# Performance work log

Hardware: AMD Instinct MI355X
Metric: run time of the kernel (lower is better)

The kernel has to match this reference:

```python
import jax, jax.numpy as jnp
import numpy as np

B, P, K, H, C = 8, 4096, 20, 64, 40  # clouds, points/cloud, knn k, hidden_feat, num_classes
NEG = 0.2  # LeakyReLU negative slope used by the repo MLP


def setup_inputs() -> dict:
    key = jax.random.key(0)
    ks = jax.random.split(key, 16)
    w = lambda k, shape: (jax.random.normal(k, shape, jnp.float32) / np.sqrt(shape[0]))
    return {
        "x": jax.random.normal(ks[0], (B * P, 3), jnp.float32),
        "batch": jnp.repeat(jnp.arange(B, dtype=jnp.int32), P),
        "W1": w(ks[1], (2 * 3, H)), "b1": jnp.zeros((H,), jnp.float32),
        "W2": w(ks[2], (2 * H, H)), "b2": jnp.zeros((H,), jnp.float32),
        "W3": w(ks[3], (2 * H, H)), "b3": jnp.zeros((H,), jnp.float32),
        "Wl": w(ks[4], (3 * H, 1024)), "bl": jnp.zeros((1024,), jnp.float32),
        "Wm1": w(ks[5], (1024, 256)), "bm1": jnp.zeros((256,), jnp.float32),
        "Wm2": w(ks[6], (256, 128)), "bm2": jnp.zeros((128,), jnp.float32),
        "Wo": w(ks[7], (128, C)), "bo": jnp.zeros((C,), jnp.float32),
    }


def _knn_idx(x):
    # x: [B,P,d] -> indices of K nearest neighbors (excluding self): [B,P,K]
    d2 = jnp.sum(x * x, axis=-1)  # [B,P]
    dist = d2[:, :, None] + d2[:, None, :] - 2.0 * jnp.einsum('bpd,bqd->bpq', x, x)
    dist = dist + jnp.eye(x.shape[1], dtype=x.dtype) * 1e10  # mask self-loops
    return jax.lax.top_k(-dist, K)[1]


def _edge_conv(x, W, b):
    # DynamicEdgeConv with max aggregation: nn([x_i, x_j - x_i]) maxed over K neighbors
    idx = _knn_idx(x)                                    # [B,P,K]
    x_j = jax.vmap(lambda xb, ib: xb[ib])(x, idx)        # [B,P,K,d]
    x_i = jnp.broadcast_to(x[:, :, None, :], x_j.shape)  # [B,P,K,d]
    feat = jnp.concatenate([x_i, x_j - x_i], axis=-1)    # [B,P,K,2d]
    h = jax.nn.leaky_relu(feat @ W + b, NEG)             # [B,P,K,H]
    return jnp.max(h, axis=2)                            # [B,P,H]


def reference(x, batch, W1, b1, W2, b2, W3, b3, Wl, bl, Wm1, bm1, Wm2, bm2, Wo, bo):
    # batch is sorted with equal-size clouds -> reshape to [B,P,3]
    xb = x.reshape(B, P, 3)
    x1 = _edge_conv(xb, W1, b1)
    x2 = _edge_conv(x1, W2, b2)
    x3 = _edge_conv(x2, W3, b3)
    h = jnp.concatenate([x1, x2, x3], axis=-1)           # [B,P,3H]
    h = jax.nn.leaky_relu(h @ Wl + bl, NEG)
    h = jax.nn.leaky_relu(h @ Wm1 + bm1, NEG)            # dropout = identity (eval)
    h = jax.nn.leaky_relu(h @ Wm2 + bm2, NEG)
    out = h @ Wo + bo                                    # [B,P,C]
    return jax.nn.log_softmax(out, axis=-1).reshape(B * P, C)
```

## Files before the change

### kernel.cpp

```cpp
#include <hip/hip_runtime.h>
#include <cstddef>
#include <cstdint>

constexpr int B_ = 8, P_ = 4096, K_ = 20, H_ = 64, C_ = 40;
constexpr int NPT = B_ * P_;
#define NEG_SLOPE 0.2f

typedef unsigned long long u64;
typedef unsigned int u32;
typedef unsigned short u16;
typedef __attribute__((ext_vector_type(8))) short bf16x8;
typedef __attribute__((ext_vector_type(4))) float f32x4;

__device__ inline u16 f2bf(float v) {
    u32 bits = __float_as_uint(v);
    return (u16)((bits + 0x7FFFu + ((bits >> 16) & 1)) >> 16);
}
__device__ inline float bf2f(u16 h) { return __uint_as_float((u32)h << 16); }

__device__ __forceinline__ void bubble20f(float (&a)[K_], float key) {
    float carry = key;
#pragma unroll
    for (int s = 0; s < K_; ++s) {
        float as = a[s];
        a[s]  = fminf(carry, as);
        carry = fmaxf(carry, as);
    }
}
__device__ __forceinline__ float mkkey(float dist, int cid) {
    return __uint_as_float((__float_as_uint(dist) & 0xFFFFF000u) | (u32)cid);
}

template <int D>
__global__ __launch_bounds__(256) void d2_kernel(const float* __restrict__ x,
                                                 float* __restrict__ d2) {
    int i = blockIdx.x * 256 + threadIdx.x;
    if (i >= NPT) return;
    const float* r = x + (size_t)i * D;
    float s = 0.f;
#pragma unroll
    for (int d = 0; d < D; ++d) { float v = r[d]; s += v * v; }
    d2[i] = s;
}

__global__ __launch_bounds__(256) void d2cvt2_kernel(const float* __restrict__ x,
                                                     float* __restrict__ d2,
                                                     u16* __restrict__ xh,
                                                     u16* __restrict__ xm) {
    int i = blockIdx.x * 256 + threadIdx.x;
    if (i >= NPT) return;
    const float* r = x + (size_t)i * 64;
    float s = 0.f;
#pragma unroll
    for (int d8 = 0; d8 < 64; d8 += 8) {
        float4 v0 = *(const float4*)(r + d8);
        float4 v1 = *(const float4*)(r + d8 + 4);
        s += v0.x * v0.x + v0.y * v0.y + v0.z * v0.z + v0.w * v0.w;
        s += v1.x * v1.x + v1.y * v1.y + v1.z * v1.z + v1.w * v1.w;
        float av[8] = {v0.x, v0.y, v0.z, v0.w, v1.x, v1.y, v1.z, v1.w};
        bf16x8 vh, vm;
#pragma unroll
        for (int j = 0; j < 8; ++j) {
            u16 h = f2bf(av[j]);
            float r1 = av[j] - bf2f(h);
            vh[j] = (short)h; vm[j] = (short)f2bf(r1);
        }
        *(bf16x8*)(xh + (size_t)i * 64 + d8) = vh;
        *(bf16x8*)(xm + (size_t)i * 64 + d8) = vm;
    }
    d2[i] = s;
}

__global__ __launch_bounds__(256) void knnf3_kernel(const float* __restrict__ x,
                                                    const float* __restrict__ d2,
                                                    int* __restrict__ idx) {
    __shared__ float sC[64][4];

    int b = blockIdx.y;
    int q0 = blockIdx.x * 64;
    const float* xc  = x + (size_t)b * P_ * 3;
    const float* d2b = d2 + (size_t)b * P_;

    int t = threadIdx.x, w = t >> 6, ln = t & 63;
    int q  = ln & 15;
    int ss = ln >> 4;

    int qrow = q0 + w * 16 + q;
    float qx = xc[(size_t)qrow * 3];
    float qy = xc[(size_t)qrow * 3 + 1];
    float qz = xc[(size_t)qrow * 3 + 2];
    float qd2 = d2b[qrow];

    float a[K_];
#pragma unroll
    for (int s = 0; s < K_; ++s)
        a[s] = __uint_as_float(0x7F7FF000u | (u32)s);
    const float PINV = __uint_as_float(0x7F800000u);
    const float BIGF = __uint_as_float(0x7F7FFFFFu);

    float p0 = PINV, p1 = PINV, p2 = PINV, p3 = PINV;
    int pcnt = 0;
    float kthr = BIGF;

    int scc = t >> 2, scm = t & 3;

#pragma unroll 1
    for (int c0 = 0; c0 < P_; c0 += 64) {
        __syncthreads();
        sC[scc][scm] = (scm < 3) ? xc[(size_t)(c0 + scc) * 3 + scm] : d2b[c0 + scc];
        __syncthreads();

#pragma unroll
        for (int nt = 0; nt < 4; ++nt) {
#pragma unroll
            for (int r = 0; r < 4; ++r) {
                int cl = nt * 16 + ss * 4 + r;
                int cID = c0 + cl;
                float4 cv = *(const float4*)&sC[cl][0];
                float dv = (qd2 + cv.w) - 2.f * (qx * cv.x + qy * cv.y + qz * cv.z);
                if (cID == qrow) dv += 1e10f;
                dv = fmaxf(dv, 0.f);
                if (__any(dv <= kthr)) {
                    float key = mkkey(dv, cID);
                    bool pass = key < a[K_ - 1];
                    p3 = pass ? p2 : p3;
                    p2 = pass ? p1 : p2;
                    p1 = pass ? p0 : p1;
                    p0 = pass ? key : p0;
                    pcnt = pass ? pcnt + 1 : pcnt;
                    if (__any(pcnt >= 4)) {
                        bubble20f(a, p3); bubble20f(a, p2); bubble20f(a, p1); bubble20f(a, p0);
                        p0 = p1 = p2 = p3 = PINV; pcnt = 0;
                        kthr = __uint_as_float(__float_as_uint(a[K_ - 1]) | 0xFFFu);
                    }
                }
            }
        }
    }
    bubble20f(a, p3); bubble20f(a, p2); bubble20f(a, p1); bubble20f(a, p0);

    int* op = idx + ((size_t)(b * P_ + qrow)) * K_;
#pragma unroll 1
    for (int k = 0; k < K_; ++k) {
        float v = a[0];
        float v1 = __shfl_xor(v, 16);
        v = fminf(v, v1);
        float v2 = __shfl_xor(v, 32);
        v = fminf(v, v2);
        bool win = (__float_as_uint(a[0]) == __float_as_uint(v));
#pragma unroll
        for (int s = 0; s < K_ - 1; ++s) a[s] = win ? a[s + 1] : a[s];
        a[K_ - 1] = win ? BIGF : a[K_ - 1];
        if (ss == 0)
            op[k] = b * P_ + (int)(__float_as_uint(v) & 0xFFFu);
    }
}

__global__ __launch_bounds__(256) void knnm64_kernel(const u16* __restrict__ xh,
                                                     const u16* __restrict__ xm,
                                                     const float* __restrict__ d2,
                                                     int* __restrict__ idx) {
    __shared__ u16 sH[64 * 64];
    __shared__ u16 sM[64 * 64];
    __shared__ float sd2[P_];

    int b = blockIdx.y;
    int q0 = blockIdx.x * 64;
    const u16* xhb = xh + (size_t)b * P_ * 64;
    const u16* xmb = xm + (size_t)b * P_ * 64;
    const float* d2b = d2 + (size_t)b * P_;

    int t = threadIdx.x, w = t >> 6, ln = t & 63;
    int q  = ln & 15;
    int ss = ln >> 4;

    for (int i = t; i < P_ / 4; i += 256)
        ((float4*)sd2)[i] = ((const float4*)d2b)[i];

    int qrow = q0 + w * 16 + q;
    bf16x8 qh[2], qm[2];
#pragma unroll
    for (int kt = 0; kt < 2; ++kt) {
        size_t off = (size_t)qrow * 64 + kt * 32 + ss * 8;
        qh[kt] = *(const bf16x8*)(xhb + off);
        qm[kt] = *(const bf16x8*)(xmb + off);
    }

    __syncthreads();
    float qd2 = sd2[qrow];

    float a[K_];
#pragma unroll
    for (int s = 0; s < K_; ++s)
        a[s] = __uint_as_float(0x7F7FF000u | (u32)s);
    const float PINV = __uint_as_float(0x7F800000u);
    const float BIGF = __uint_as_float(0x7F7FFFFFu);

    float p0 = PINV, p1 = PINV, p2 = PINV, p3 = PINV;
    int pcnt = 0;
    float kthr = BIGF;

    int sr = t >> 2;
    int sk2 = (t & 3) * 32;
    int sbase = sr * 128, sswz = (sr & 7) << 4;
    size_t sgof = (size_t)sr * 64 + (t & 3) * 16;

#pragma unroll 1
    for (int c0 = 0; c0 < P_; c0 += 64) {
        __syncthreads();
        {
            size_t g = (size_t)c0 * 64 + sgof;
            bf16x8 h0 = *(const bf16x8*)(xhb + g);
            bf16x8 h1 = *(const bf16x8*)(xhb + g + 8);
            bf16x8 m0 = *(const bf16x8*)(xmb + g);
            bf16x8 m1 = *(const bf16x8*)(xmb + g + 8);
            *(bf16x8*)((char*)sH + sbase + (sk2 ^ sswz)) = h0;
            *(bf16x8*)((char*)sH + sbase + ((sk2 + 16) ^ sswz)) = h1;
            *(bf16x8*)((char*)sM + sbase + (sk2 ^ sswz)) = m0;
            *(bf16x8*)((char*)sM + sbase + ((sk2 + 16) ^ sswz)) = m1;
        }
        __syncthreads();

        f32x4 acc[4];
#pragma unroll
        for (int nt = 0; nt < 4; ++nt) {
            acc[nt] = (f32x4){0.f, 0.f, 0.f, 0.f};
            int r = nt * 16 + q;
            int base = r * 128, swz = (r & 7) << 4;
#pragma unroll
            for (int kt = 0; kt < 2; ++kt) {
                int k2 = kt * 64 + ss * 16;
                bf16x8 ch = *(const bf16x8*)((char*)sH + base + (k2 ^ swz));
                bf16x8 cm = *(const bf16x8*)((char*)sM + base + (k2 ^ swz));
                acc[nt] = __builtin_amdgcn_mfma_f32_16x16x32_bf16(cm, qh[kt], acc[nt], 0, 0, 0);
                acc[nt] = __builtin_amdgcn_mfma_f32_16x16x32_bf16(ch, qm[kt], acc[nt], 0, 0, 0);
                acc[nt] = __builtin_amdgcn_mfma_f32_16x16x32_bf16(ch, qh[kt], acc[nt], 0, 0, 0);
            }
        }

        float dvv[4][4];
        float mn = 3.4e38f;
#pragma unroll
        for (int nt = 0; nt < 4; ++nt) {
#pragma unroll
            for (int r = 0; r < 4; ++r) {
                int cID = c0 + nt * 16 + ss * 4 + r;
                float dv = (qd2 + sd2[cID]) - 2.f * acc[nt][r];
                if (cID == qrow) dv += 1e10f;
                dv = fmaxf(dv, 0.f);
                dvv[nt][r] = dv;
                mn = fminf(mn, dv);
            }
        }
        if (__any(mn <= kthr)) {
#pragma unroll
            for (int nt = 0; nt < 4; ++nt) {
#pragma unroll
                for (int r = 0; r < 4; ++r) {
                    float dv = dvv[nt][r];
                    if (__any(dv <= kthr)) {
                        float key = mkkey(dv, c0 + nt * 16 + ss * 4 + r);
                        bool pass = key < a[K_ - 1];
                        p3 = pass ? p2 : p3;
                        p2 = pass ? p1 : p2;
                        p1 = pass ? p0 : p1;
                        p0 = pass ? key : p0;
                        pcnt = pass ? pcnt + 1 : pcnt;
                        if (__any(pcnt >= 4)) {
                            bubble20f(a, p3); bubble20f(a, p2); bubble20f(a, p1); bubble20f(a, p0);
                            p0 = p1 = p2 = p3 = PINV; pcnt = 0;
                            kthr = __uint_as_float(__float_as_uint(a[K_ - 1]) | 0xFFFu);
                        }
                    }
                }
            }
        }
    }
    bubble20f(a, p3); bubble20f(a, p2); bubble20f(a, p1); bubble20f(a, p0);

    int* op = idx + ((size_t)(b * P_ + qrow)) * K_;
#pragma unroll 1
    for (int k = 0; k < K_; ++k) {
        float v = a[0];
        float v1 = __shfl_xor(v, 16);
        v = fminf(v, v1);
        float v2 = __shfl_xor(v, 32);
        v = fminf(v, v2);
        bool win = (__float_as_uint(a[0]) == __float_as_uint(v));
#pragma unroll
        for (int s = 0; s < K_ - 1; ++s) a[s] = win ? a[s + 1] : a[s];
        a[K_ - 1] = win ? BIGF : a[K_ - 1];
        if (ss == 0)
            op[k] = b * P_ + (int)(__float_as_uint(v) & 0xFFFu);
    }
}

__global__ __launch_bounds__(256) void prep_kernel(const float* __restrict__ W2,
                                                   const float* __restrict__ b2,
                                                   const float* __restrict__ W3,
                                                   const float* __restrict__ b3,
                                                   const float* __restrict__ Wl,
                                                   const float* __restrict__ Wm1,
                                                   const float* __restrict__ Wm2,
                                                   float* __restrict__ Wpk2, float* __restrict__ bpk2,
                                                   float* __restrict__ Wpk3, float* __restrict__ bpk3,
                                                   u16* __restrict__ WlT,
                                                   u16* __restrict__ Wm1T,
                                                   u16* __restrict__ Wm2T) {
    int t = blockIdx.x * 256 + threadIdx.x;
    if (t < 8192) {
        int d = t >> 7, h2 = t & 127;
        Wpk2[t] = (h2 < 64) ? W2[d * 64 + h2] : W2[(64 + d) * 64 + (h2 - 64)];
        if (t < 128) bpk2[t] = (t < 64) ? b2[t] : 0.f;
    } else if (t < 16384) {
        int t2 = t - 8192;
        int d = t2 >> 7, h2 = t2 & 127;
        Wpk3[t2] = (h2 < 64) ? W3[d * 64 + h2] : W3[(64 + d) * 64 + (h2 - 64)];
        if (t2 < 128) bpk3[t2] = (t2 < 64) ? b3[t2] : 0.f;
    } else if (t < 212992) {
        int t2 = t - 16384;
        int k = t2 >> 10, n = t2 & 1023;
        WlT[(size_t)n * 192 + k] = f2bf(Wl[t2]);
    } else if (t < 475136) {
        int t2 = t - 212992;
        int k = t2 >> 8, n = t2 & 255;
        Wm1T[(size_t)n * 1024 + k] = f2bf(Wm1[t2]);
    } else if (t < 507904) {
        int t2 = t - 475136;
        int k = t2 >> 7, n = t2 & 127;
        Wm2T[(size_t)n * 256 + k] = f2bf(Wm2[t2]);
    }
}

__global__ __launch_bounds__(256) void uv3_kernel(const float* __restrict__ x,
                                                  const float* __restrict__ W,
                                                  const float* __restrict__ b,
                                                  float* __restrict__ UV) {
    int t = blockIdx.x * 256 + threadIdx.x;
    int p = t >> 7, h2 = t & 127;
    float x0 = x[p * 3], x1 = x[p * 3 + 1], x2 = x[p * 3 + 2];
    float r;
    if (h2 < 64) {
        r = b[h2] + x0 * W[h2] + x1 * W[64 + h2] + x2 * W[128 + h2];
    } else {
        int h = h2 - 64;
        r = x0 * W[192 + h] + x1 * W[256 + h] + x2 * W[320 + h];
    }
    UV[t] = r;
}

__global__ __launch_bounds__(256) void edgemax_kernel(const float* __restrict__ UV,
                                                      const int* __restrict__ idx,
                                                      float* __restrict__ xout) {
    int wv = threadIdx.x >> 6, lane = threadIdx.x & 63;
    int p = blockIdx.x * 4 + wv;
    const float* uvp = UV + (size_t)p * 128;
    float duv = uvp[lane] - uvp[64 + lane];
    const int* ip = idx + (size_t)p * K_;
    int jj[K_];
#pragma unroll
    for (int k = 0; k < K_; ++k) jj[k] = ip[k];
    float m = -3.4e38f;
#pragma unroll
    for (int k = 0; k < K_; ++k) {
        float vj = UV[(size_t)jj[k] * 128 + 64 + lane];
        float t = duv + vj;
        m = fmaxf(m, fmaxf(t, NEG_SLOPE * t));
    }
    xout[(size_t)p * H_ + lane] = m;
}

__global__ __launch_bounds__(256) void gemm_kernel(const float* __restrict__ A1,
                                                   const float* __restrict__ Wm,
                                                   const float* __restrict__ bias,
                                                   float* __restrict__ Cm,
                                                   int M, int N, int Kd, int leaky) {
    __shared__ float sA[32][68];
    __shared__ float sB[32][68];

    int tid = threadIdx.x;
    int row0 = blockIdx.x * 64, col0 = blockIdx.y * 64;
    int tx = tid & 15, ty = tid >> 4;

    int lr  = tid >> 2;
    int lk4 = (tid & 3) * 4;
    int lkb = tid >> 4;
    int lnb = (tid & 15) * 4;

    float acc[4][4] = {};

    for (int k0 = 0; k0 < Kd; k0 += 32) {
        int arow = row0 + lr;
#pragma unroll
        for (int h = 0; h < 32; h += 16) {
            int kk = k0 + lk4 + h;
            const float* src = A1 + (size_t)arow * Kd + kk;
            float4 av = *(const float4*)src;
            sA[lk4 + h + 0][lr] = av.x; sA[lk4 + h + 1][lr] = av.y;
            sA[lk4 + h + 2][lr] = av.z; sA[lk4 + h + 3][lr] = av.w;
        }
        int bcol = col0 + lnb;
#pragma unroll
        for (int h = 0; h < 32; h += 16) {
            float4 bv = make_float4(0.f, 0.f, 0.f, 0.f);
            if (bcol < N) bv = *(const float4*)(Wm + (size_t)(k0 + lkb + h) * N + bcol);
            *(float4*)&sB[lkb + h][lnb] = bv;
        }
        __syncthreads();

#pragma unroll
        for (int kk2 = 0; kk2 < 32; ++kk2) {
            float4 a = *(const float4*)&sA[kk2][ty * 4];
            float4 bb = *(const float4*)&sB[kk2][tx * 4];
            acc[0][0] = fmaf(a.x, bb.x, acc[0][0]); acc[0][1] = fmaf(a.x, bb.y, acc[0][1]);
            acc[0][2] = fmaf(a.x, bb.z, acc[0][2]); acc[0][3] = fmaf(a.x, bb.w, acc[0][3]);
            acc[1][0] = fmaf(a.y, bb.x, acc[1][0]); acc[1][1] = fmaf(a.y, bb.y, acc[1][1]);
            acc[1][2] = fmaf(a.y, bb.z, acc[1][2]); acc[1][3] = fmaf(a.y, bb.w, acc[1][3]);
            acc[2][0] = fmaf(a.z, bb.x, acc[2][0]); acc[2][1] = fmaf(a.z, bb.y, acc[2][1]);
            acc[2][2] = fmaf(a.z, bb.z, acc[2][2]); acc[2][3] = fmaf(a.z, bb.w, acc[2][3]);
            acc[3][0] = fmaf(a.w, bb.x, acc[3][0]); acc[3][1] = fmaf(a.w, bb.y, acc[3][1]);
            acc[3][2] = fmaf(a.w, bb.z, acc[3][2]); acc[3][3] = fmaf(a.w, bb.w, acc[3][3]);
        }
        __syncthreads();
    }

    for (int i = 0; i < 4; ++i) {
        int row = row0 + ty * 4 + i;
        for (int j = 0; j < 4; ++j) {
            int col = col0 + tx * 4 + j;
            if (col < N) {
                float v = acc[i][j] + bias[col];
                if (leaky) v = v > 0.f ? v : NEG_SLOPE * v;
                Cm[(size_t)row * N + col] = v;
            }
        }
    }
}

template <int KD, int OUT_BF16>
__global__ __launch_bounds__(256) void gemm_mfma_kernel(const u16* __restrict__ A,
                                                        const u16* __restrict__ BT,
                                                        const float* __restrict__ bias,
                                                        void* __restrict__ Cout,
                                                        int N, int leaky) {
    __shared__ u16 sA[128 * 64];
    __shared__ u16 sB[128 * 64];

    int t = threadIdx.x;
    int wave = t >> 6, lane = t & 63;
    int wm = wave >> 1, wn = wave & 1;
    int row0 = blockIdx.x * 128;
    int col0 = blockIdx.y * 128;

    f32x4 acc[4][4] = {};

    for (int k0 = 0; k0 < KD; k0 += 64) {
        __syncthreads();
#pragma unroll
        for (int i = 0; i < 4; ++i) {
            int li = t + i * 256;
            int r = li >> 3;
            int kc = (li & 7) * 8;
            bf16x8 v = *(const bf16x8*)(A + (size_t)(row0 + r) * KD + k0 + kc);
            *(bf16x8*)((char*)sA + r * 128 + ((kc * 2) ^ ((r & 7) << 4))) = v;
        }
#pragma unroll
        for (int i = 0; i < 4; ++i) {
            int li = t + i * 256;
            int n = li >> 3;
            int kc = (li & 7) * 8;
            bf16x8 v = *(const bf16x8*)(BT + (size_t)(col0 + n) * KD + k0 + kc);
            *(bf16x8*)((char*)sB + n * 128 + ((kc * 2) ^ ((n & 7) << 4))) = v;
        }
        __syncthreads();

#pragma unroll
        for (int kk = 0; kk < 2; ++kk) {
            int kb = kk * 64 + (lane >> 4) * 16;
            bf16x8 af[4], bfr[4];
#pragma unroll
            for (int mi = 0; mi < 4; ++mi) {
                int r = wm * 64 + mi * 16 + (lane & 15);
                af[mi] = *(const bf16x8*)((char*)sA + r * 128 + (kb ^ ((r & 7) << 4)));
            }
#pragma unroll
            for (int ni = 0; ni < 4; ++ni) {
                int n = wn * 64 + ni * 16 + (lane & 15);
                bfr[ni] = *(const bf16x8*)((char*)sB + n * 128 + (kb ^ ((n & 7) << 4)));
            }
#pragma unroll
            for (int mi = 0; mi < 4; ++mi)
#pragma unroll
                for (int ni = 0; ni < 4; ++ni)
                    acc[mi][ni] = __builtin_amdgcn_mfma_f32_16x16x32_bf16(
                        af[mi], bfr[ni], acc[mi][ni], 0, 0, 0);
        }
    }

#pragma unroll
    for (int ni = 0; ni < 4; ++ni) {
        int col = col0 + wn * 64 + ni * 16 + (lane & 15);
        float bs = bias[col];
#pragma unroll
        for (int mi = 0; mi < 4; ++mi) {
#pragma unroll
            for (int r = 0; r < 4; ++r) {
                int row = row0 + wm * 64 + mi * 16 + (lane >> 4) * 4 + r;
                float v = acc[mi][ni][r] + bs;
                if (leaky) v = v > 0.f ? v : NEG_SLOPE * v;
                if (OUT_BF16)
                    ((u16*)Cout)[(size_t)row * N + col] = f2bf(v);
                else
                    ((float*)Cout)[(size_t)row * N + col] = v;
            }
        }
    }
}

__global__ __launch_bounds__(256) void gemm_mfma_cat_kernel(const float* __restrict__ x1,
                                                            const float* __restrict__ x2,
                                                            const float* __restrict__ x3,
                                                            const u16* __restrict__ BT,
                                                            const float* __restrict__ bias,
                                                            u16* __restrict__ Cout,
                                                            int N) {
    __shared__ u16 sA[128 * 64];
    __shared__ u16 sB[128 * 64];

    int t = threadIdx.x;
    int wave = t >> 6, lane = t & 63;
    int wm = wave >> 1, wn = wave & 1;
    int row0 = blockIdx.x * 128;
    int col0 = blockIdx.y * 128;

    f32x4 acc[4][4] = {};

#pragma unroll 1
    for (int k0 = 0; k0 < 192; k0 += 64) {
        const float* src = (k0 == 0) ? x1 : (k0 == 64) ? x2 : x3;
        __syncthreads();
#pragma unroll
        for (int i = 0; i < 4; ++i) {
            int li = t + i * 256;
            int r = li >> 3;
            int kc = (li & 7) * 8;
            const float* sp = src + (size_t)(row0 + r) * 64 + kc;
            float4 a0 = *(const float4*)sp;
            float4 a1 = *(const float4*)(sp + 4);
            bf16x8 v;
            v[0] = (short)f2bf(a0.x); v[1] = (short)f2bf(a0.y);
            v[2] = (short)f2bf(a0.z); v[3] = (short)f2bf(a0.w);
            v[4] = (short)f2bf(a1.x); v[5] = (short)f2bf(a1.y);
            v[6] = (short)f2bf(a1.z); v[7] = (short)f2bf(a1.w);
            *(bf16x8*)((char*)sA + r * 128 + ((kc * 2) ^ ((r & 7) << 4))) = v;
        }
#pragma unroll
        for (int i = 0; i < 4; ++i) {
            int li = t + i * 256;
            int n = li >> 3;
            int kc = (li & 7) * 8;
            bf16x8 v = *(const bf16x8*)(BT + (size_t)(col0 + n) * 192 + k0 + kc);
            *(bf16x8*)((char*)sB + n * 128 + ((kc * 2) ^ ((n & 7) << 4))) = v;
        }
        __syncthreads();

#pragma unroll
        for (int kk = 0; kk < 2; ++kk) {
            int kb = kk * 64 + (lane >> 4) * 16;
            bf16x8 af[4], bfr[4];
#pragma unroll
            for (int mi = 0; mi < 4; ++mi) {
                int r = wm * 64 + mi * 16 + (lane & 15);
                af[mi] = *(const bf16x8*)((char*)sA + r * 128 + (kb ^ ((r & 7) << 4)));
            }
#pragma unroll
            for (int ni = 0; ni < 4; ++ni) {
                int n = wn * 64 + ni * 16 + (lane & 15);
                bfr[ni] = *(const bf16x8*)((char*)sB + n * 128 + (kb ^ ((n & 7) << 4)));
            }
#pragma unroll
            for (int mi = 0; mi < 4; ++mi)
#pragma unroll
                for (int ni = 0; ni < 4; ++ni)
                    acc[mi][ni] = __builtin_amdgcn_mfma_f32_16x16x32_bf16(
                        af[mi], bfr[ni], acc[mi][ni], 0, 0, 0);
        }
    }

#pragma unroll
    for (int ni = 0; ni < 4; ++ni) {
        int col = col0 + wn * 64 + ni * 16 + (lane & 15);
        float bs = bias[col];
#pragma unroll
        for (int mi = 0; mi < 4; ++mi) {
#pragma unroll
            for (int r = 0; r < 4; ++r) {
                int row = row0 + wm * 64 + mi * 16 + (lane >> 4) * 4 + r;
                float v = acc[mi][ni][r] + bs;
                v = v > 0.f ? v : NEG_SLOPE * v;
                Cout[(size_t)row * N + col] = f2bf(v);
            }
        }
    }
}

__global__ __launch_bounds__(256) void lsm_wo_kernel(const float* __restrict__ act3,
                                                     const float* __restrict__ Wo,
                                                     const float* __restrict__ bo,
                                                     float* __restrict__ out) {
    __shared__ float sWo[128 * 44];
    __shared__ float sAct[4][128];

    int t = threadIdx.x;
    for (int i = t; i < 128 * 40; i += 256) {
        int k = i / 40, c = i % 40;
        sWo[k * 44 + c] = Wo[i];
    }
    __syncthreads();

    int wv = t >> 6, lane = t & 63;
    int row = blockIdx.x * 4 + wv;
    sAct[wv][lane]      = act3[(size_t)row * 128 + lane];
    sAct[wv][64 + lane] = act3[(size_t)row * 128 + 64 + lane];

    float acc = (lane < C_) ? bo[lane] : -3.4e38f;
    if (lane < C_) {
#pragma unroll 8
        for (int k = 0; k < 128; ++k)
            acc = fmaf(sAct[wv][k], sWo[k * 44 + lane], acc);
    }
    float m = acc;
#pragma unroll
    for (int s = 1; s < 64; s <<= 1) m = fmaxf(m, __shfl_xor(m, s));
    float e = (lane < C_) ? expf(acc - m) : 0.f;
    float sum = e;
#pragma unroll
    for (int s = 1; s < 64; s <<= 1) sum += __shfl_xor(sum, s);
    if (lane < C_) out[(size_t)row * C_ + lane] = acc - m - logf(sum);
}

extern "C" void kernel_launch(void* const* d_in, const int* in_sizes, int n_in,
                              void* d_out, int out_size, void* d_ws, size_t ws_size,
                              hipStream_t stream) {
    const float* x   = (const float*)d_in[0];
    const float* W1  = (const float*)d_in[2];
    const float* b1  = (const float*)d_in[3];
    const float* W2  = (const float*)d_in[4];
    const float* b2  = (const float*)d_in[5];
    const float* W3  = (const float*)d_in[6];
    const float* b3  = (const float*)d_in[7];
    const float* Wl  = (const float*)d_in[8];
    const float* bl  = (const float*)d_in[9];
    const float* Wm1 = (const float*)d_in[10];
    const float* bm1 = (const float*)d_in[11];
    const float* Wm2 = (const float*)d_in[12];
    const float* bm2 = (const float*)d_in[13];
    const float* Wo  = (const float*)d_in[14];
    const float* bo  = (const float*)d_in[15];
    float* out = (float*)d_out;

    char* ws = (char*)d_ws;
    float* x1   = (float*)(ws);
    float* x2   = (float*)(ws + 8388608);
    float* x3   = (float*)(ws + 16777216);
    int*   idx  = (int*)  (ws + 25165824);
    float* d2   = (float*)(ws + 27787264);
    char* hb = ws + 27918336;
    u16*   xhs  = (u16*)(hb);
    u16*   xms  = (u16*)(hb + 4194304);
    float* UV   = (float*)(hb);
    float* Wpk2 = (float*)(ws + 44695552);
    float* bpk2 = (float*)(ws + 44728320);
    float* Wpk3 = (float*)(ws + 44728832);
    float* bpk3 = (float*)(ws + 44761600);
    u16*   WlT  = (u16*)  (ws + 44762112);
    u16*   Wm1T = (u16*)  (ws + 45155328);
    u16*   Wm2T = (u16*)  (ws + 45679616);
    u16*   act1 = (u16*)(hb);
    u16*   act2 = (u16*)(ws + 45745152);
    float* act3 = (float*)(hb);

    prep_kernel<<<1984, 256, 0, stream>>>(W2, b2, W3, b3, Wl, Wm1, Wm2,
                                          Wpk2, bpk2, Wpk3, bpk3, WlT, Wm1T, Wm2T);

    d2_kernel<3><<<NPT / 256, 256, 0, stream>>>(x, d2);
    knnf3_kernel<<<dim3(P_ / 64, B_), 256, 0, stream>>>(x, d2, idx);
    uv3_kernel<<<NPT * 128 / 256, 256, 0, stream>>>(x, W1, b1, UV);
    edgemax_kernel<<<NPT / 4, 256, 0, stream>>>(UV, idx, x1);
    d2cvt2_kernel<<<NPT / 256, 256, 0, stream>>>(x1, d2, xhs, xms);
    knnm64_kernel<<<dim3(P_ / 64, B_), 256, 0, stream>>>(xhs, xms, d2, idx);
    gemm_kernel<<<dim3(NPT / 64, 2), 256, 0, stream>>>(x1, Wpk2, bpk2, UV, NPT, 128, 64, 0);
    edgemax_kernel<<<NPT / 4, 256, 0, stream>>>(UV, idx, x2);
    d2cvt2_kernel<<<NPT / 256, 256, 0, stream>>>(x2, d2, xhs, xms);
    knnm64_kernel<<<dim3(P_ / 64, B_), 256, 0, stream>>>(xhs, xms, d2, idx);
    gemm_kernel<<<dim3(NPT / 64, 2), 256, 0, stream>>>(x2, Wpk3, bpk3, UV, NPT, 128, 64, 0);
    edgemax_kernel<<<NPT / 4, 256, 0, stream>>>(UV, idx, x3);

    for (int c = 0; c < 4; ++c) {
        size_t r0 = (size_t)c * 8192;
        gemm_mfma_cat_kernel<<<dim3(64, 8), 256, 0, stream>>>(x1 + r0 * 64, x2 + r0 * 64,
                                                              x3 + r0 * 64, WlT, bl, act1, 1024);
        gemm_mfma_kernel<1024, 1><<<dim3(64, 2), 256, 0, stream>>>(act1, Wm1T, bm1, act2, 256, 1);
        gemm_mfma_kernel<256, 0><<<dim3(64, 1), 256, 0, stream>>>(act2, Wm2T, bm2, act3, 128, 1);
        lsm_wo_kernel<<<2048, 256, 0, stream>>>(act3, Wo, bo, out + r0 * C_);
    }
}
```

Before: 897.5 us.

## Fuse Wm2 GEMM with output head and inline squared norms in kNN kernels

The Wm2 MFMA GEMM is merged with the Wo projection and log-softmax into one tail kernel, which keeps the 128-wide activation in shared memory instead of writing and rereading act3 through global memory. The separate d2 kernel for the 3-D input is dropped, and knnf3 now computes squared norms inline. knnm64 no longer stages the whole 4096-entry d2 array in shared memory per block and instead loads 64 norms per candidate tile, which reduces LDS use and could allow higher occupancy. The risk is that the tail kernel launches only 128 blocks per chunk and reads Wm2T directly from global memory for each wave, so it may be underutilized.

```diff
diff --git a/kernel.cpp b/kernel.cpp
--- a/kernel.cpp
+++ b/kernel.cpp
@@ -29,18 +29,6 @@
 }
 __device__ __forceinline__ float mkkey(float dist, int cid) {
     return __uint_as_float((__float_as_uint(dist) & 0xFFFFF000u) | (u32)cid);
-}
-
-template <int D>
-__global__ __launch_bounds__(256) void d2_kernel(const float* __restrict__ x,
-                                                 float* __restrict__ d2) {
-    int i = blockIdx.x * 256 + threadIdx.x;
-    if (i >= NPT) return;
-    const float* r = x + (size_t)i * D;
-    float s = 0.f;
-#pragma unroll
-    for (int d = 0; d < D; ++d) { float v = r[d]; s += v * v; }
-    d2[i] = s;
 }
 
 __global__ __launch_bounds__(256) void d2cvt2_kernel(const float* __restrict__ x,
@@ -72,14 +60,12 @@
 }
 
 __global__ __launch_bounds__(256) void knnf3_kernel(const float* __restrict__ x,
-                                                    const float* __restrict__ d2,
                                                     int* __restrict__ idx) {
     __shared__ float sC[64][4];
 
     int b = blockIdx.y;
     int q0 = blockIdx.x * 64;
-    const float* xc  = x + (size_t)b * P_ * 3;
-    const float* d2b = d2 + (size_t)b * P_;
+    const float* xc = x + (size_t)b * P_ * 3;
 
     int t = threadIdx.x, w = t >> 6, ln = t & 63;
     int q  = ln & 15;
@@ -89,7 +75,7 @@
     float qx = xc[(size_t)qrow * 3];
     float qy = xc[(size_t)qrow * 3 + 1];
     float qz = xc[(size_t)qrow * 3 + 2];
-    float qd2 = d2b[qrow];
+    float qd2 = qx * qx + qy * qy + qz * qz;
 
     float a[K_];
 #pragma unroll
@@ -107,7 +93,14 @@
 #pragma unroll 1
     for (int c0 = 0; c0 < P_; c0 += 64) {
         __syncthreads();
-        sC[scc][scm] = (scm < 3) ? xc[(size_t)(c0 + scc) * 3 + scm] : d2b[c0 + scc];
+        if (scm < 3) {
+            sC[scc][scm] = xc[(size_t)(c0 + scc) * 3 + scm];
+        } else {
+            float ax = xc[(size_t)(c0 + scc) * 3];
+            float ay = xc[(size_t)(c0 + scc) * 3 + 1];
+            float az = xc[(size_t)(c0 + scc) * 3 + 2];
+            sC[scc][3] = ax * ax + ay * ay + az * az;
+        }
         __syncthreads();
 
 #pragma unroll
@@ -162,7 +155,7 @@
                                                      int* __restrict__ idx) {
     __shared__ u16 sH[64 * 64];
     __shared__ u16 sM[64 * 64];
-    __shared__ float sd2[P_];
+    __shared__ float sCd2[64];
 
     int b = blockIdx.y;
     int q0 = blockIdx.x * 64;
@@ -174,9 +167,6 @@
     int q  = ln & 15;
     int ss = ln >> 4;
 
-    for (int i = t; i < P_ / 4; i += 256)
-        ((float4*)sd2)[i] = ((const float4*)d2b)[i];
-
     int qrow = q0 + w * 16 + q;
     bf16x8 qh[2], qm[2];
 #pragma unroll
@@ -185,9 +175,7 @@
         qh[kt] = *(const bf16x8*)(xhb + off);
         qm[kt] = *(const bf16x8*)(xmb + off);
     }
-
-    __syncthreads();
-    float qd2 = sd2[qrow];
+    float qd2 = d2b[qrow];
 
     float a[K_];
 #pragma unroll
@@ -218,6 +206,7 @@
             *(bf16x8*)((char*)sH + sbase + ((sk2 + 16) ^ sswz)) = h1;
             *(bf16x8*)((char*)sM + sbase + (sk2 ^ sswz)) = m0;
             *(bf16x8*)((char*)sM + sbase + ((sk2 + 16) ^ sswz)) = m1;
+            if (t < 64) sCd2[t] = d2b[c0 + t];
         }
         __syncthreads();
 
@@ -244,9 +233,9 @@
         for (int nt = 0; nt < 4; ++nt) {
 #pragma unroll
             for (int r = 0; r < 4; ++r) {
-                int cID = c0 + nt * 16 + ss * 4 + r;
-                float dv = (qd2 + sd2[cID]) - 2.f * acc[nt][r];
-                if (cID == qrow) dv += 1e10f;
+                int cl = nt * 16 + ss * 4 + r;
+                float dv = (qd2 + sCd2[cl]) - 2.f * acc[nt][r];
+                if (c0 + cl == qrow) dv += 1e10f;
                 dv = fmaxf(dv, 0.f);
                 dvv[nt][r] = dv;
                 mn = fminf(mn, dv);
@@ -604,39 +593,66 @@
     }
 }
 
-__global__ __launch_bounds__(256) void lsm_wo_kernel(const float* __restrict__ act3,
-                                                     const float* __restrict__ Wo,
-                                                     const float* __restrict__ bo,
-                                                     float* __restrict__ out) {
+__global__ __launch_bounds__(256) void tail_kernel(const u16* __restrict__ act2,
+                                                   const u16* __restrict__ Wm2T,
+                                                   const float* __restrict__ bm2,
+                                                   const float* __restrict__ Wo,
+                                                   const float* __restrict__ bo,
+                                                   float* __restrict__ out) {
+    __shared__ float sAct[64][132];
     __shared__ float sWo[128 * 44];
-    __shared__ float sAct[4][128];
-
-    int t = threadIdx.x;
+
+    int t = threadIdx.x, w = t >> 6, lane = t & 63;
+    int row0 = blockIdx.x * 64;
+
     for (int i = t; i < 128 * 40; i += 256) {
         int k = i / 40, c = i % 40;
         sWo[k * 44 + c] = Wo[i];
     }
+
+    int arow = row0 + w * 16 + (lane & 15);
+    bf16x8 af[8];
+#pragma unroll
+    for (int kt = 0; kt < 8; ++kt)
+        af[kt] = *(const bf16x8*)(act2 + (size_t)arow * 256 + kt * 32 + (lane >> 4) * 8);
+
+#pragma unroll
+    for (int ni = 0; ni < 8; ++ni) {
+        f32x4 acc = (f32x4){0.f, 0.f, 0.f, 0.f};
+        int n = ni * 16 + (lane & 15);
+#pragma unroll
+        for (int kt = 0; kt < 8; ++kt) {
+            bf16x8 bf = *(const bf16x8*)(Wm2T + (size_t)n * 256 + kt * 32 + (lane >> 4) * 8);
+            acc = __builtin_amdgcn_mfma_f32_16x16x32_bf16(af[kt], bf, acc, 0, 0, 0);
+        }
+        float bs = bm2[n];
+#pragma unroll
+        for (int r = 0; r < 4; ++r) {
+            float v = acc[r] + bs;
+            v = v > 0.f ? v : NEG_SLOPE * v;
+            sAct[w * 16 + (lane >> 4) * 4 + r][n] = v;
+        }
+    }
     __syncthreads();
 
-    int wv = t >> 6, lane = t & 63;
-    int row = blockIdx.x * 4 + wv;
-    sAct[wv][lane]      = act3[(size_t)row * 128 + lane];
-    sAct[wv][64 + lane] = act3[(size_t)row * 128 + 64 + lane];
-
-    float acc = (lane < C_) ? bo[lane] : -3.4e38f;
-    if (lane < C_) {
+#pragma unroll 1
+    for (int rr = 0; rr < 16; ++rr) {
+        int lrow = w * 16 + rr;
+        float accv = (lane < C_) ? bo[lane] : -3.4e38f;
+        if (lane < C_) {
 #pragma unroll 8
-        for (int k = 0; k < 128; ++k)
-            acc = fmaf(sAct[wv][k], sWo[k * 44 + lane], acc);
-    }
-    float m = acc;
-#pragma unroll
-    for (int s = 1; s < 64; s <<= 1) m = fmaxf(m, __shfl_xor(m, s));
-    float e = (lane < C_) ? expf(acc - m) : 0.f;
-    float sum = e;
-#pragma unroll
-    for (int s = 1; s < 64; s <<= 1) sum += __shfl_xor(sum, s);
-    if (lane < C_) out[(size_t)row * C_ + lane] = acc - m - logf(sum);
+            for (int k = 0; k < 128; ++k)
+                accv = fmaf(sAct[lrow][k], sWo[k * 44 + lane], accv);
+        }
+        float m = accv;
+#pragma unroll
+        for (int s = 1; s < 64; s <<= 1) m = fmaxf(m, __shfl_xor(m, s));
+        float e = (lane < C_) ? expf(accv - m) : 0.f;
+        float sum = e;
+#pragma unroll
+        for (int s = 1; s < 64; s <<= 1) sum += __shfl_xor(sum, s);
+        if (lane < C_) out[(size_t)(row0 + lrow) * C_ + lane] = accv - m - logf(sum);
+    }
 }
 
 extern "C" void kernel_launch(void* const* d_in, const int* in_sizes, int n_in,
@@ -678,13 +694,11 @@
     u16*   Wm2T = (u16*)  (ws + 45679616);
     u16*   act1 = (u16*)(hb);
     u16*   act2 = (u16*)(ws + 45745152);
-    float* act3 = (float*)(hb);
 
     prep_kernel<<<1984, 256, 0, stream>>>(W2, b2, W3, b3, Wl, Wm1, Wm2,
                                           Wpk2, bpk2, Wpk3, bpk3, WlT, Wm1T, Wm2T);
 
-    d2_kernel<3><<<NPT / 256, 256, 0, stream>>>(x, d2);
-    knnf3_kernel<<<dim3(P_ / 64, B_), 256, 0, stream>>>(x, d2, idx);
+    knnf3_kernel<<<dim3(P_ / 64, B_), 256, 0, stream>>>(x, idx);
     uv3_kernel<<<NPT * 128 / 256, 256, 0, stream>>>(x, W1, b1, UV);
     edgemax_kernel<<<NPT / 4, 256, 0, stream>>>(UV, idx, x1);
     d2cvt2_kernel<<<NPT / 256, 256, 0, stream>>>(x1, d2, xhs, xms);
@@ -701,7 +715,6 @@
         gemm_mfma_cat_kernel<<<dim3(64, 8), 256, 0, stream>>>(x1 + r0 * 64, x2 + r0 * 64,
                                                               x3 + r0 * 64, WlT, bl, act1, 1024);
         gemm_mfma_kernel<1024, 1><<<dim3(64, 2), 256, 0, stream>>>(act1, Wm1T, bm1, act2, 256, 1);
-        gemm_mfma_kernel<256, 0><<<dim3(64, 1), 256, 0, stream>>>(act2, Wm2T, bm2, act3, 128, 1);
-        lsm_wo_kernel<<<2048, 256, 0, stream>>>(act3, Wo, bo, out + r0 * C_);
-    }
-}
+        tail_kernel<<<128, 256, 0, stream>>>(act2, Wm2T, bm2, Wo, bo, out + r0 * C_);
+    }
+}
```

Measured after the change: 991.4 us. 10.5% more time.
